# Performance work log

Measured on AMD Instinct MI355X. Metric: run time of the kernel, lower is better.

## Reference

```python
import jax, jax.numpy as jnp
import numpy as np

SEGMENT_LENGTHS = [1024, 2048, 4096]
DILATION_RATES = [1, 2, 4]


def _head_groups(num_heads, num_segments):
    base = num_heads // num_segments
    extra = num_heads % num_segments
    groups = [base] * num_segments
    for i in range(extra):
        groups[-(i + 1)] += 1
    return groups


def _dilated_indices(segment_len, dilation_rate, offset):
    # Mirrors RingDilatedAttentionV2._apply_dilation index construction (static).
    if dilation_rate > 1:
        idx = np.arange(offset, segment_len, dilation_rate)
        repeats = (segment_len + len(idx) - 1) // len(idx)
        idx = np.tile(idx, repeats)[:segment_len] % segment_len
    else:
        idx = np.arange(segment_len)
    return jnp.asarray(idx, dtype=jnp.int32)


def setup_inputs() -> dict:
    key = jax.random.key(0)
    kq, kk, kv = jax.random.split(key, 3)
    b, n, h, d = 1, 4096, 12, 64
    return {
        "query": jax.random.normal(kq, (b, n, h, d), dtype=jnp.float32),
        "key": jax.random.normal(kk, (b, n, h, d), dtype=jnp.float32),
        "value": jax.random.normal(kv, (b, n, h, d), dtype=jnp.float32),
        "is_causal": 1,
    }


def _dilated_attention(query, key, value, is_causal):
    b, n, h, d = query.shape
    groups = _head_groups(h, len(SEGMENT_LENGTHS))
    scale = 1.0 / np.sqrt(d).astype(np.float32)
    outs = []
    head_start = 0
    for i, (seg_len, rate, g) in enumerate(zip(SEGMENT_LENGTHS, DILATION_RATES, groups)):
        if g == 0:
            continue
        sl = min(seg_len, n)
        ns = n // sl  # n chosen divisible by every segment length
        q = query[:, :, head_start:head_start + g, :].reshape(b, ns, sl, g, d)
        k = key[:, :, head_start:head_start + g, :].reshape(b, ns, sl, g, d)
        v = value[:, :, head_start:head_start + g, :].reshape(b, ns, sl, g, d)
        if rate > 1 or i > 0:
            idx = _dilated_indices(sl, rate, i)
            k = k[:, :, idx]
            v = v[:, :, idx]
        # scores: [b, seg, heads, q_pos, k_pos]
        scores = jnp.einsum("bsqhd,bskhd->bshqk", q, k) * scale
        if is_causal:
            causal = jnp.triu(jnp.ones((sl, sl), dtype=bool), k=1)
            scores = jnp.where(causal, jnp.finfo(scores.dtype).min, scores)
        attn = jax.nn.softmax(scores, axis=-1)
        o = jnp.einsum("bshqk,bskhd->bsqhd", attn, v).reshape(b, n, g, d)
        outs.append(o)
        head_start += g
    return jnp.concatenate(outs, axis=2)  # [b, n, h, d]


def reference(query, key, value, is_causal):
    return _dilated_attention(query, key, value, is_causal)
```

## Files before the change

### kernel.cpp

```cpp
#include <hip/hip_runtime.h>
#include <hip/hip_bf16.h>
#include <math.h>

typedef __bf16 bf16x8 __attribute__((ext_vector_type(8)));
typedef float  f32x4  __attribute__((ext_vector_type(4)));
typedef float  f32x16 __attribute__((ext_vector_type(16)));
typedef int    int2v  __attribute__((ext_vector_type(2)));
typedef unsigned int uint4v __attribute__((ext_vector_type(4)));
typedef unsigned short ushort_t;

#define LDK 72

#define KG_OFF  0
#define VGT_OFF 6291456
#define LACC_OFF 12582912
#define CTR_OFF  12779520

#define N_ITEMS 1536

__device__ __forceinline__ int gather_pos(int gi, int group) {
    const int lsl = 10 + group;
    const int seg = gi >> lsl;
    const int j   = gi - (seg << lsl);
    return (seg << lsl) + group + ((j & 1023) << group);
}

__device__ __forceinline__ void gld_lds16(const ushort_t* g, __bf16* l) {
    __builtin_amdgcn_global_load_lds(
        (const __attribute__((address_space(1))) void*)g,
        (__attribute__((address_space(3))) void*)l, 16, 0, 0);
}

__device__ __forceinline__ unsigned int pk_bf16(float lo, float hi) {
    unsigned short a = __builtin_bit_cast(unsigned short, (__bf16)lo);
    unsigned short b = __builtin_bit_cast(unsigned short, (__bf16)hi);
    return ((unsigned int)b << 16) | (unsigned int)a;
}

__device__ __forceinline__ f32x16 zero16() {
    f32x16 z;
    #pragma unroll
    for (int i = 0; i < 16; ++i) z[i] = 0.f;
    return z;
}

__global__ __launch_bounds__(256)
void preconvert_kernel(const float* __restrict__ K, const float* __restrict__ V,
                       ushort_t* __restrict__ Kg, ushort_t* __restrict__ VgT,
                       float* __restrict__ Out, float* __restrict__ l_acc,
                       int* __restrict__ ctr)
{
    const int HD = 768;
    int b = blockIdx.x;
    const int tid = threadIdx.x;
    if (b < 768) {
        if (b == 0 && tid == 0) *ctr = 0;
        {
            float4 z = {0.f, 0.f, 0.f, 0.f};
            float4* zp = (float4*)Out + ((size_t)b * 256 + tid) * 4;
            zp[0] = z; zp[1] = z; zp[2] = z; zp[3] = z;
        }
        const int h = b % 12, gi0 = (b / 12) * 64;
        const int group = h >> 2;
        const int gi = gi0 + (tid >> 2);
        const int d0 = (tid & 3) << 4;
        const int pos = gather_pos(gi, group);
        const float* kp = K + (size_t)pos * HD + h * 64 + d0;
        float4 x0 = ((const float4*)kp)[0], x1 = ((const float4*)kp)[1];
        float4 x2 = ((const float4*)kp)[2], x3 = ((const float4*)kp)[3];
        bf16x8 w0, w1;
        w0[0]=(__bf16)x0.x; w0[1]=(__bf16)x0.y; w0[2]=(__bf16)x0.z; w0[3]=(__bf16)x0.w;
        w0[4]=(__bf16)x1.x; w0[5]=(__bf16)x1.y; w0[6]=(__bf16)x1.z; w0[7]=(__bf16)x1.w;
        w1[0]=(__bf16)x2.x; w1[1]=(__bf16)x2.y; w1[2]=(__bf16)x2.z; w1[3]=(__bf16)x2.w;
        w1[4]=(__bf16)x3.x; w1[5]=(__bf16)x3.y; w1[6]=(__bf16)x3.z; w1[7]=(__bf16)x3.w;
        ushort_t* out = Kg + ((size_t)(h * 4096 + gi)) * 64 + d0;
        *(bf16x8*)out = w0;
        *(bf16x8*)(out + 8) = w1;
    } else {
        b -= 768;
        if (b < 192) l_acc[b * 256 + tid] = 0.f;
        const int h = b % 12, gi0 = (b / 12) * 64;
        const int group = h >> 2;
        __shared__ __align__(16) __bf16 Ts[64 * LDK];
        const int gil = tid >> 2;
        const int d0 = (tid & 3) << 4;
        const int pos = gather_pos(gi0 + gil, group);
        const float* vp = V + (size_t)pos * HD + h * 64 + d0;
        float4 x0 = ((const float4*)vp)[0], x1 = ((const float4*)vp)[1];
        float4 x2 = ((const float4*)vp)[2], x3 = ((const float4*)vp)[3];
        bf16x8 w0, w1;
        w0[0]=(__bf16)x0.x; w0[1]=(__bf16)x0.y; w0[2]=(__bf16)x0.z; w0[3]=(__bf16)x0.w;
        w0[4]=(__bf16)x1.x; w0[5]=(__bf16)x1.y; w0[6]=(__bf16)x1.z; w0[7]=(__bf16)x1.w;
        w1[0]=(__bf16)x2.x; w1[1]=(__bf16)x2.y; w1[2]=(__bf16)x2.z; w1[3]=(__bf16)x2.w;
        w1[4]=(__bf16)x3.x; w1[5]=(__bf16)x3.y; w1[6]=(__bf16)x3.z; w1[7]=(__bf16)x3.w;
        *(bf16x8*)&Ts[gil * LDK + d0]     = w0;
        *(bf16x8*)&Ts[gil * LDK + d0 + 8] = w1;
        __syncthreads();
        const int d = tid >> 2, c = tid & 3;
        bf16x8 o0, o1;
        #pragma unroll
        for (int i = 0; i < 8; ++i) {
            o0[i] = Ts[(c * 16 + i) * LDK + d];
            o1[i] = Ts[(c * 16 + 8 + i) * LDK + d];
        }
        ushort_t* out = VgT + ((size_t)(h * 64 + d)) * 4096 + gi0 + c * 16;
        *(bf16x8*)out = o0;
        *(bf16x8*)(out + 8) = o1;
    }
}

__global__ __launch_bounds__(256)
void dilated_attn_kernel(const float* __restrict__ Q,
                         const ushort_t* __restrict__ Kg,
                         const ushort_t* __restrict__ VgT,
                         const int* __restrict__ is_causal_p,
                         float* __restrict__ Out,
                         float* __restrict__ l_acc,
                         int* __restrict__ ctr)
{
    const int HD = 768;
    const int causal = (*is_causal_p) != 0;

    const int tid  = threadIdx.x;
    const int wave = tid >> 6;
    const int lane = tid & 63;
    const int l31  = lane & 31;
    const int hi   = lane >> 5;

    __shared__ __align__(16) __bf16 Ks[2][64 * 64];
    __shared__ __align__(16) __bf16 Vs[2][64 * 64];
    __shared__ int s_item;

    const int bx16 = (((lane & 7) ^ (lane >> 3)) & 7) << 3;
    const int r8   = lane >> 3;

    for (;;) {
        if (tid == 0) s_item = atomicAdd(ctr, 1);
        __syncthreads();
        const int bx = s_item;
        __syncthreads();
        if (bx >= N_ITEMS) break;

        const int qt  = 31 - (bx / 48);
        const int rem = bx % 48;
        const int h   = rem % 12;
        const int c   = rem / 12;
        const int group = h >> 2;
        const int sl    = 1024 << group;

        const int q0 = qt << 7;
        const int qb = q0 & (sl - 1);
        const int seg_start = q0 - qb;
        const int blk_diag = (qb + 127) >> 6;
        const int nkt = causal ? (blk_diag + 1) : (sl >> 6);
        const int kt0 = c << 4;
        if (kt0 >= nkt) continue;
        const int kend = min(kt0 + 16, nkt);
        const int nch  = (nkt + 15) >> 4;

        const ushort_t* kg_head = Kg + (size_t)h * 4096 * 64;
        const ushort_t* vt_head = VgT + (size_t)h * 64 * 4096;

        auto stage = [&](int kt, int buf) {
            const ushort_t* kb = kg_head + ((size_t)(seg_start + (kt << 6)) << 6);
            const ushort_t* vb = vt_head + seg_start + (kt << 6);
            #pragma unroll
            for (int i = 0; i < 2; ++i) {
                const int row = i * 32 + wave * 8 + r8;
                gld_lds16(kb + row * 64 + bx16, &Ks[buf][(i * 32 + wave * 8) * 64]);
                gld_lds16(vb + (size_t)row * 4096 + bx16, &Vs[buf][(i * 32 + wave * 8) * 64]);
            }
        };

        stage(kt0, 0);

        const int qrow = q0 + wave * 32 + l31;
        const float* qptr = Q + (size_t)qrow * HD + h * 64;
        bf16x8 qf[4];
        {
            const float s = 0.125f * 1.4426950408889634f;
            #pragma unroll
            for (int ds = 0; ds < 4; ++ds) {
                float4 x0 = ((const float4*)(qptr + ds * 16 + hi * 8))[0];
                float4 x1 = ((const float4*)(qptr + ds * 16 + hi * 8))[1];
                bf16x8 w;
                w[0]=(__bf16)(x0.x*s); w[1]=(__bf16)(x0.y*s); w[2]=(__bf16)(x0.z*s); w[3]=(__bf16)(x0.w*s);
                w[4]=(__bf16)(x1.x*s); w[5]=(__bf16)(x1.y*s); w[6]=(__bf16)(x1.z*s); w[7]=(__bf16)(x1.w*s);
                qf[ds] = w;
            }
        }

        const int mydiag = causal ? ((qb + wave * 32 + 31) >> 6) : 0x7fffffff;
        const int lrow   = ((wave & 1) << 5) + l31;

        f32x16 o0 = zero16(), o1 = zero16();
        float l_part = 0.f;

        for (int kt = kt0; kt < kend; ++kt) {
            const int cur = (kt - kt0) & 1;

            asm volatile("s_waitcnt vmcnt(0)" ::: "memory");
            __builtin_amdgcn_s_barrier();
            __builtin_amdgcn_sched_barrier(0);

            if (kt + 1 < kend) stage(kt + 1, cur ^ 1);

            if (kt <= mydiag) {
                f32x16 s0 = zero16(), s1 = zero16();
                const int xr = (l31 & 7);
                __builtin_amdgcn_s_setprio(1);
                #pragma unroll
                for (int ds = 0; ds < 4; ++ds) {
                    const int cb = ds * 2 + hi;
                    bf16x8 k0 = *(const bf16x8*)&Ks[cur][l31 * 64        + ((cb ^ xr) << 3)];
                    bf16x8 k1 = *(const bf16x8*)&Ks[cur][(32 + l31) * 64 + ((cb ^ xr) << 3)];
                    s0 = __builtin_amdgcn_mfma_f32_32x32x16_bf16(k0, qf[ds], s0, 0, 0, 0);
                    s1 = __builtin_amdgcn_mfma_f32_32x32x16_bf16(k1, qf[ds], s1, 0, 0, 0);
                }
                __builtin_amdgcn_s_setprio(0);

                float p[2][16];
                const bool isdiag = causal && (kt == mydiag);
                #pragma unroll
                for (int r = 0; r < 16; ++r) {
                    float v0 = __builtin_amdgcn_exp2f(s0[r]);
                    float v1 = __builtin_amdgcn_exp2f(s1[r]);
                    if (isdiag) {
                        const int kl = (r & 3) + ((r >> 2) << 3) + (hi << 2);
                        if (kl > lrow)      v0 = 0.f;
                        if (kl + 32 > lrow) v1 = 0.f;
                    }
                    p[0][r] = v0; p[1][r] = v1;
                    l_part += v0 + v1;
                }

                __builtin_amdgcn_s_setprio(1);
                #pragma unroll
                for (int b = 0; b < 2; ++b) {
                    #pragma unroll
                    for (int ks2 = 0; ks2 < 2; ++ks2) {
                        const int g = ks2 * 8;
                        int x0 = (int)pk_bf16(p[b][g + 0], p[b][g + 1]);
                        int x1 = (int)pk_bf16(p[b][g + 2], p[b][g + 3]);
                        int y0 = (int)pk_bf16(p[b][g + 4], p[b][g + 5]);
                        int y1 = (int)pk_bf16(p[b][g + 6], p[b][g + 7]);
                        int2v r02 = __builtin_amdgcn_permlane32_swap(x0, y0, false, false);
                        int2v r13 = __builtin_amdgcn_permlane32_swap(x1, y1, false, false);
                        uint4v t;
                        t[0] = (unsigned int)r02[0];
                        t[1] = (unsigned int)r13[0];
                        t[2] = (unsigned int)r02[1];
                        t[3] = (unsigned int)r13[1];
                        bf16x8 pa = __builtin_bit_cast(bf16x8, t);
                        const int kcb = (b * 2 + ks2) * 2 + hi;
                        bf16x8 v0 = *(const bf16x8*)&Vs[cur][l31 * 64        + ((kcb ^ xr) << 3)];
                        bf16x8 v1 = *(const bf16x8*)&Vs[cur][(32 + l31) * 64 + ((kcb ^ xr) << 3)];
                        o0 = __builtin_amdgcn_mfma_f32_32x32x16_bf16(pa, v0, o0, 0, 0, 0);
                        o1 = __builtin_amdgcn_mfma_f32_32x32x16_bf16(pa, v1, o1, 0, 0, 0);
                    }
                }
                __builtin_amdgcn_s_setprio(0);
            }
        }

        const float l2 = l_part + __shfl_xor(l_part, 32);
        const int qw = q0 + wave * 32;
        if (nch == 1) {
            const float inv = 1.0f / l2;
            #pragma unroll
            for (int r = 0; r < 16; ++r) {
                const int qloc = (r & 3) + ((r >> 2) << 3) + (hi << 2);
                const float invq = __shfl(inv, qloc);
                const int row = qw + qloc;
                Out[(size_t)row * HD + h * 64 + l31]      = o0[r] * invq;
                Out[(size_t)row * HD + h * 64 + 32 + l31] = o1[r] * invq;
            }
        } else {
            if (hi == 0) atomicAdd(&l_acc[(qw + l31) * 12 + h], l2);
            #pragma unroll
            for (int r = 0; r < 16; ++r) {
                const int qloc = (r & 3) + ((r >> 2) << 3) + (hi << 2);
                const int row = qw + qloc;
                atomicAdd(&Out[(size_t)row * HD + h * 64 + l31],      o0[r]);
                atomicAdd(&Out[(size_t)row * HD + h * 64 + 32 + l31], o1[r]);
            }
        }
    }
}

__global__ __launch_bounds__(256)
void finalize_kernel(float* __restrict__ Out, const float* __restrict__ l_acc,
                     const int* __restrict__ is_causal_p)
{
    const int causal = (*is_causal_p) != 0;
    const int idx = blockIdx.x * 256 + threadIdx.x;
    const int rh = idx >> 4;
    const int d4 = idx & 15;
    const int h = rh % 12;
    const int row = rh / 12;
    const int group = h >> 2;
    const int ntf = 16 << group;
    const int qt128 = row >> 7;
    const int qb_t = (qt128 << 1) & (ntf - 1);
    const int nkt = causal ? (qb_t + 2) : ntf;
    if (nkt <= 16) return;
    const float inv = 1.0f / l_acc[rh];
    float4* p = (float4*)Out + (size_t)rh * 16 + d4;
    float4 v = *p;
    v.x *= inv; v.y *= inv; v.z *= inv; v.w *= inv;
    *p = v;
}

extern "C" void kernel_launch(void* const* d_in, const int* in_sizes, int n_in,
                              void* d_out, int out_size, void* d_ws, size_t ws_size,
                              hipStream_t stream) {
    (void)in_sizes; (void)n_in; (void)out_size; (void)ws_size;
    const float* Q = (const float*)d_in[0];
    const float* K = (const float*)d_in[1];
    const float* V = (const float*)d_in[2];
    const int* isc = (const int*)d_in[3];
    float* Out = (float*)d_out;
    ushort_t* Kg   = (ushort_t*)((char*)d_ws + KG_OFF);
    ushort_t* VgT  = (ushort_t*)((char*)d_ws + VGT_OFF);
    float*    lacc = (float*)((char*)d_ws + LACC_OFF);
    int*      ctr  = (int*)((char*)d_ws + CTR_OFF);

    preconvert_kernel<<<1536, 256, 0, stream>>>(K, V, Kg, VgT, Out, lacc, ctr);
    dilated_attn_kernel<<<1280, 256, 0, stream>>>(Q, Kg, VgT, isc, Out, lacc, ctr);
    finalize_kernel<<<3072, 256, 0, stream>>>(Out, lacc, isc);
}
```

Before: 143.9 us.

## Schedule work items longest-first via constexpr table and shrink persistent grid

Replaces the fixed linear work-item enumeration with a compile-time table in constant memory that lists only non-empty (q-tile, head, chunk) items, sorted by descending number of K tiles. This removes wasted atomic fetches on skipped items and improves load balance by handing out the most expensive items first. The persistent grid shrinks from 1280 to 512 blocks, which means fewer concurrent blocks and possibly lower occupancy in exchange for less contention on the counter.

```diff
diff --git a/kernel.cpp b/kernel.cpp
--- a/kernel.cpp
+++ b/kernel.cpp
@@ -16,7 +16,32 @@
 #define LACC_OFF 12582912
 #define CTR_OFF  12779520
 
-#define N_ITEMS 1536
+struct ItemTab { unsigned short v[896]; int n; };
+
+constexpr ItemTab build_items(int causal) {
+    ItemTab t{};
+    for (int i = 0; i < 896; ++i) t.v[i] = 0xFFFF;
+    t.n = 0;
+    for (int cost = 16; cost >= 1; --cost)
+        for (int qt = 31; qt >= 0; --qt)
+            for (int h = 11; h >= 0; --h) {
+                const int group = h >> 2;
+                const int sl = 1024 << group;
+                const int qb = (qt << 7) & (sl - 1);
+                const int nkt = causal ? (((qb + 127) >> 6) + 1) : (sl >> 6);
+                for (int c = 0; c < 4; ++c) {
+                    const int kt0 = c << 4;
+                    if (kt0 >= nkt) continue;
+                    const int rem = nkt - kt0;
+                    const int cst = rem < 16 ? rem : 16;
+                    if (cst == cost) t.v[t.n++] = (unsigned short)((qt << 6) | (h << 2) | c);
+                }
+            }
+    return t;
+}
+
+__constant__ ItemTab g_tab_c = build_items(1);
+__constant__ ItemTab g_tab_n = build_items(0);
 
 __device__ __forceinline__ int gather_pos(int gi, int group) {
     const int lsl = 10 + group;
@@ -120,6 +145,8 @@
 {
     const int HD = 768;
     const int causal = (*is_causal_p) != 0;
+    const ItemTab& tab = causal ? g_tab_c : g_tab_n;
+    const int n_items = tab.n;
 
     const int tid  = threadIdx.x;
     const int wave = tid >> 6;
@@ -137,14 +164,14 @@
     for (;;) {
         if (tid == 0) s_item = atomicAdd(ctr, 1);
         __syncthreads();
-        const int bx = s_item;
+        const int n = s_item;
         __syncthreads();
-        if (bx >= N_ITEMS) break;
-
-        const int qt  = 31 - (bx / 48);
-        const int rem = bx % 48;
-        const int h   = rem % 12;
-        const int c   = rem / 12;
+        if (n >= n_items) break;
+
+        const int enc = tab.v[n];
+        const int qt  = enc >> 6;
+        const int h   = (enc >> 2) & 15;
+        const int c   = enc & 3;
         const int group = h >> 2;
         const int sl    = 1024 << group;
 
@@ -154,7 +181,6 @@
         const int blk_diag = (qb + 127) >> 6;
         const int nkt = causal ? (blk_diag + 1) : (sl >> 6);
         const int kt0 = c << 4;
-        if (kt0 >= nkt) continue;
         const int kend = min(kt0 + 16, nkt);
         const int nch  = (nkt + 15) >> 4;
 
@@ -326,6 +352,6 @@
     int*      ctr  = (int*)((char*)d_ws + CTR_OFF);
 
     preconvert_kernel<<<1536, 256, 0, stream>>>(K, V, Kg, VgT, Out, lacc, ctr);
-    dilated_attn_kernel<<<1280, 256, 0, stream>>>(Q, Kg, VgT, isc, Out, lacc, ctr);
+    dilated_attn_kernel<<<512, 256, 0, stream>>>(Q, Kg, VgT, isc, Out, lacc, ctr);
     finalize_kernel<<<3072, 256, 0, stream>>>(Out, lacc, isc);
 }
```

Measured after the change: 135.2 us. 6.1% less time.
